# Kernel tuning notes

Measured on AMD Instinct MI355X. Metric: run time of the kernel, lower is better.

## Reference

```python
import jax, jax.numpy as jnp
import numpy as np

B, IN, HID, OUT, E = 8192, 1024, 4096, 1024, 8
EPS = 1e-5  # torch LayerNorm default


def _layernorm(x, gamma, beta):
    # normalize over last axis; gamma/beta broadcast as [E, dim] against [B, E, dim]
    mu = jnp.mean(x, axis=-1, keepdims=True)
    var = jnp.var(x, axis=-1, keepdims=True)
    return (x - mu) * jax.lax.rsqrt(var + EPS) * gamma + beta


def setup_inputs() -> dict:
    key = jax.random.key(0)
    ks = jax.random.split(key, 8)
    x = jax.random.normal(ks[0], (B, IN), dtype=jnp.float32)
    weights = jax.random.uniform(ks[1], (B, E), dtype=jnp.float32)
    s1 = 1.0 / np.sqrt(IN)
    s2 = 1.0 / np.sqrt(HID)
    W1 = jax.random.uniform(ks[2], (E, IN, HID), minval=-s1, maxval=s1, dtype=jnp.float32)
    b1 = jax.random.uniform(ks[3], (E, HID), minval=-s1, maxval=s1, dtype=jnp.float32)
    W2 = jax.random.uniform(ks[4], (E, HID, OUT), minval=-s2, maxval=s2, dtype=jnp.float32)
    b2 = jax.random.uniform(ks[5], (E, OUT), minval=-s2, maxval=s2, dtype=jnp.float32)
    g1 = jnp.ones((E, HID), dtype=jnp.float32)
    be1 = jnp.zeros((E, HID), dtype=jnp.float32)
    g2 = jnp.ones((E, OUT), dtype=jnp.float32)
    be2 = jnp.zeros((E, OUT), dtype=jnp.float32)
    return {"x": x, "weights": weights, "W1": W1, "b1": b1, "g1": g1, "be1": be1,
            "W2": W2, "b2": b2, "g2": g2, "be2": be2}


def reference(x, weights, W1, b1, g1, be1, W2, b2, g2, be2):
    # Each expert MLP([1024,4096,1024]): Linear -> LN -> GELU -> Linear -> LN -> GELU
    # (MLP appends LayerNorm + activation after EVERY Linear, including the last).
    # Dropout p=0 / eval mode -> identity. All experts run on every token.
    h = jnp.einsum('bi,eih->beh', x, W1) + b1          # [B, E, HID]
    h = jax.nn.gelu(_layernorm(h, g1, be1), approximate=False)
    y = jnp.einsum('beh,eho->beo', h, W2) + b2         # [B, E, OUT]
    y = jax.nn.gelu(_layernorm(y, g2, be2), approximate=False)
    # weighted combine: einsum('bij,bi->bj')
    return jnp.einsum('beo,be->bo', y, weights)        # [B, OUT]
```

## Files before the change

kernel.cpp:

```cpp
#include <hip/hip_runtime.h>
#include <cstdint>
#include <cstddef>

typedef unsigned short u16;
typedef float f32x4 __attribute__((ext_vector_type(4)));
typedef __bf16 bf16x8 __attribute__((ext_vector_type(8)));

#define B_DIM   8192
#define IN_DIM  1024
#define HID_DIM 4096
#define OUT_DIM 1024
#define NEXP    8

__device__ __forceinline__ u16 f2b(float f) {
    uint32_t u = __builtin_bit_cast(uint32_t, f);
    u += 0x7fffu + ((u >> 16) & 1u);
    return (u16)(u >> 16);
}
__device__ __forceinline__ float b2f(u16 b) {
    uint32_t u = ((uint32_t)b) << 16;
    return __builtin_bit_cast(float, u);
}
__device__ __forceinline__ float gelu_fast(float x) {
    float y = x * (0.7978845608f + 0.03567740814f * x * x);
    float a = fminf(y * 2.8853900818f, 80.0f);
    float e = __builtin_amdgcn_exp2f(a);
    return x * e * __builtin_amdgcn_rcpf(e + 1.0f);
}
__device__ __forceinline__ void async_cp16(const void* g, void* l) {
    __builtin_amdgcn_global_load_lds(
        (const __attribute__((address_space(1))) void*)g,
        (__attribute__((address_space(3))) void*)l,
        16, 0, 0);
}

__global__ __launch_bounds__(256)
void cvt_bf16(const float* __restrict__ in, u16* __restrict__ out, int n4) {
    int i = blockIdx.x * 256 + threadIdx.x;
    if (i >= n4) return;
    float4 v = *(const float4*)&in[(size_t)i * 4];
    uint2 o;
    o.x = (uint32_t)f2b(v.x) | ((uint32_t)f2b(v.y) << 16);
    o.y = (uint32_t)f2b(v.z) | ((uint32_t)f2b(v.w) << 16);
    *(uint2*)&out[(size_t)i * 4] = o;
}

__global__ __launch_bounds__(256)
void transpose_cvt2(const float* __restrict__ W1e, u16* __restrict__ w1t,
                    const float* __restrict__ W2e, u16* __restrict__ w2t) {
    __shared__ float tile[32][33];
    const float* W; u16* Wt; int K, N, n0, k0;
    if (blockIdx.z == 0) {
        W = W1e; Wt = w1t; K = IN_DIM; N = HID_DIM;
        n0 = blockIdx.x * 32; k0 = blockIdx.y * 32;
    } else {
        W = W2e; Wt = w2t; K = HID_DIM; N = OUT_DIM;
        n0 = blockIdx.y * 32; k0 = blockIdx.x * 32;
    }
    const int tx = threadIdx.x & 31, ty = threadIdx.x >> 5;
#pragma unroll
    for (int i = 0; i < 4; ++i) {
        int k = k0 + ty + i * 8;
        tile[ty + i * 8][tx] = W[(size_t)k * N + n0 + tx];
    }
    __syncthreads();
#pragma unroll
    for (int i = 0; i < 4; ++i) {
        int n = n0 + ty + i * 8;
        Wt[(size_t)n * K + k0 + tx] = f2b(tile[tx][ty + i * 8]);
    }
}

__global__ __launch_bounds__(256)
void gemm_bt_bias(const u16* __restrict__ A, const u16* __restrict__ Bt,
                  const float* __restrict__ bias, u16* __restrict__ C,
                  int M, int N, int K) {
    __shared__ __attribute__((aligned(16))) u16 sA[2][128 * 32];
    __shared__ __attribute__((aligned(16))) u16 sB[2][128 * 32];

    const int tid  = threadIdx.x;
    const int wid  = tid >> 6;
    const int lane = tid & 63;
    const int quad = lane >> 4;
    const int lr   = lane & 15;
    const int wm   = wid & 1;
    const int wn   = wid >> 1;

    const int NX = gridDim.x, NY = gridDim.y;
    const int bid = blockIdx.y * NX + blockIdx.x;
    const int xcd = bid & 7;
    const int j   = bid >> 3;
    const int yl  = j / NX;
    const int bx  = j - yl * NX;
    const int by  = xcd * (NY >> 3) + yl;

    const int m0 = by * 128;
    const int n0 = bx * 128;

    const int sr  = lane >> 2;
    const int scl = ((lane & 3) ^ ((lane >> 3) & 3)) * 8;
    const int qsw = (lr >> 1) & 3;

    const u16* Ag = A + (size_t)m0 * K;
    const u16* Bg = Bt + (size_t)n0 * K;

    f32x4 acc[4][4] = {};

    for (int k0 = 0; k0 < K; k0 += 64) {
#pragma unroll
        for (int s = 0; s < 2; ++s) {
#pragma unroll
            for (int i = 0; i < 2; ++i) {
                const int rb = wid * 32 + i * 16;
                async_cp16(Ag + (size_t)(rb + sr) * K + k0 + s * 32 + scl,
                           &sA[s][rb * 32]);
                async_cp16(Bg + (size_t)(rb + sr) * K + k0 + s * 32 + scl,
                           &sB[s][rb * 32]);
            }
        }
        __syncthreads();

#pragma unroll
        for (int s = 0; s < 2; ++s) {
            bf16x8 af[4], bfr[4];
#pragma unroll
            for (int mi = 0; mi < 4; ++mi)
                af[mi] = *(const bf16x8*)
                    &sA[s][(wm * 64 + mi * 16 + lr) * 32 + ((quad ^ qsw) * 8)];
#pragma unroll
            for (int ni = 0; ni < 4; ++ni)
                bfr[ni] = *(const bf16x8*)
                    &sB[s][(wn * 64 + ni * 16 + lr) * 32 + ((quad ^ qsw) * 8)];

#pragma unroll
            for (int mi = 0; mi < 4; ++mi)
#pragma unroll
                for (int ni = 0; ni < 4; ++ni)
                    acc[mi][ni] = __builtin_amdgcn_mfma_f32_16x16x32_bf16(
                        af[mi], bfr[ni], acc[mi][ni], 0, 0, 0);
        }

        __syncthreads();
    }

    float bvv[4];
#pragma unroll
    for (int ni = 0; ni < 4; ++ni)
        bvv[ni] = bias[n0 + wn * 64 + ni * 16 + lr];

#pragma unroll
    for (int mi = 0; mi < 4; ++mi) {
        const int mr = m0 + wm * 64 + mi * 16 + quad * 4;
#pragma unroll
        for (int r = 0; r < 4; ++r) {
            u16* Crow = C + (size_t)(mr + r) * N + n0 + wn * 64 + lr;
#pragma unroll
            for (int ni = 0; ni < 4; ++ni)
                Crow[ni * 16] = f2b(acc[mi][ni][r] + bvv[ni]);
        }
    }
}

__global__ __launch_bounds__(256)
void ln_gelu_hid(u16* __restrict__ h, const float* __restrict__ g,
                 const float* __restrict__ be) {
    __shared__ float red[8];
    const int row = blockIdx.x;
    u16* hp = h + (size_t)row * HID_DIM;
    const int t = threadIdx.x;

    uint4 v0 = *(const uint4*)&hp[t * 8];
    uint4 v1 = *(const uint4*)&hp[(t + 256) * 8];

    float vals[16];
    {
        const uint32_t w0[4] = {v0.x, v0.y, v0.z, v0.w};
        const uint32_t w1[4] = {v1.x, v1.y, v1.z, v1.w};
#pragma unroll
        for (int q = 0; q < 4; ++q) {
            vals[q * 2]     = b2f((u16)(w0[q] & 0xffffu));
            vals[q * 2 + 1] = b2f((u16)(w0[q] >> 16));
            vals[8 + q * 2]     = b2f((u16)(w1[q] & 0xffffu));
            vals[8 + q * 2 + 1] = b2f((u16)(w1[q] >> 16));
        }
    }
    float s = 0.f, ss = 0.f;
#pragma unroll
    for (int i = 0; i < 16; ++i) { s += vals[i]; ss += vals[i] * vals[i]; }

    float4 gv[4], bv[4];
    gv[0] = *(const float4*)&g[t * 8];
    gv[1] = *(const float4*)&g[t * 8 + 4];
    gv[2] = *(const float4*)&g[(t + 256) * 8];
    gv[3] = *(const float4*)&g[(t + 256) * 8 + 4];
    bv[0] = *(const float4*)&be[t * 8];
    bv[1] = *(const float4*)&be[t * 8 + 4];
    bv[2] = *(const float4*)&be[(t + 256) * 8];
    bv[3] = *(const float4*)&be[(t + 256) * 8 + 4];

#pragma unroll
    for (int off = 32; off > 0; off >>= 1) {
        s += __shfl_down(s, off, 64);
        ss += __shfl_down(ss, off, 64);
    }
    if ((t & 63) == 0) { red[(t >> 6) * 2] = s; red[(t >> 6) * 2 + 1] = ss; }
    __syncthreads();
    s  = red[0] + red[2] + red[4] + red[6];
    ss = red[1] + red[3] + red[5] + red[7];
    const float mean = s * (1.f / HID_DIM);
    const float rstd = rsqrtf(ss * (1.f / HID_DIM) - mean * mean + 1e-5f);

    const float* gf = (const float*)gv;
    const float* bf = (const float*)bv;
#pragma unroll
    for (int j = 0; j < 2; ++j) {
        uint4 o;
        uint32_t* ow = (uint32_t*)&o;
#pragma unroll
        for (int q = 0; q < 4; ++q) {
            const int k = j * 8 + q * 2;
            float u0 = gelu_fast((vals[k]     - mean) * rstd * gf[k]     + bf[k]);
            float u1 = gelu_fast((vals[k + 1] - mean) * rstd * gf[k + 1] + bf[k + 1]);
            ow[q] = (uint32_t)f2b(u0) | ((uint32_t)f2b(u1) << 16);
        }
        *(uint4*)&hp[(t + j * 256) * 8] = o;
    }
}

__global__ __launch_bounds__(256)
void ln_gelu_combine(const u16* __restrict__ y, const float* __restrict__ g,
                     const float* __restrict__ be, const float* __restrict__ wts,
                     float* __restrict__ out, int e, int first) {
    __shared__ float red[8];
    const int row = blockIdx.x;
    const u16* yp = y + (size_t)row * OUT_DIM;
    const int t = threadIdx.x;

    uint2 v = *(const uint2*)&yp[t * 4];
    float f0 = b2f((u16)(v.x & 0xffffu)), f1 = b2f((u16)(v.x >> 16));
    float f2 = b2f((u16)(v.y & 0xffffu)), f3 = b2f((u16)(v.y >> 16));
    float s = f0 + f1 + f2 + f3;
    float ss = f0 * f0 + f1 * f1 + f2 * f2 + f3 * f3;

    const int n = t * 4;
    float4 gv = *(const float4*)&g[n];
    float4 bvv = *(const float4*)&be[n];

#pragma unroll
    for (int off = 32; off > 0; off >>= 1) {
        s += __shfl_down(s, off, 64);
        ss += __shfl_down(ss, off, 64);
    }
    if ((t & 63) == 0) { red[(t >> 6) * 2] = s; red[(t >> 6) * 2 + 1] = ss; }
    __syncthreads();
    s  = red[0] + red[2] + red[4] + red[6];
    ss = red[1] + red[3] + red[5] + red[7];
    const float mean = s * (1.f / OUT_DIM);
    const float rstd = rsqrtf(ss * (1.f / OUT_DIM) - mean * mean + 1e-5f);

    const float w = wts[(size_t)row * NEXP + e];
    float4 o;
    if (first) { o.x = o.y = o.z = o.w = 0.f; }
    else       { o = *(const float4*)&out[(size_t)row * OUT_DIM + n]; }
    o.x += w * gelu_fast((f0 - mean) * rstd * gv.x + bvv.x);
    o.y += w * gelu_fast((f1 - mean) * rstd * gv.y + bvv.y);
    o.z += w * gelu_fast((f2 - mean) * rstd * gv.z + bvv.z);
    o.w += w * gelu_fast((f3 - mean) * rstd * gv.w + bvv.w);
    *(float4*)&out[(size_t)row * OUT_DIM + n] = o;
}

extern "C" void kernel_launch(void* const* d_in, const int* in_sizes, int n_in,
                              void* d_out, int out_size, void* d_ws, size_t ws_size,
                              hipStream_t stream) {
    (void)in_sizes; (void)n_in; (void)out_size; (void)ws_size;
    const float* x   = (const float*)d_in[0];
    const float* wts = (const float*)d_in[1];
    const float* W1  = (const float*)d_in[2];
    const float* b1  = (const float*)d_in[3];
    const float* g1  = (const float*)d_in[4];
    const float* be1 = (const float*)d_in[5];
    const float* W2  = (const float*)d_in[6];
    const float* b2  = (const float*)d_in[7];
    const float* g2  = (const float*)d_in[8];
    const float* be2 = (const float*)d_in[9];
    float* out = (float*)d_out;

    char* p = (char*)d_ws;
    u16* xb  = (u16*)p; p += (size_t)B_DIM * IN_DIM * 2;
    u16* w1t = (u16*)p; p += (size_t)HID_DIM * IN_DIM * 2;
    u16* w2t = (u16*)p; p += (size_t)OUT_DIM * HID_DIM * 2;
    u16* h   = (u16*)p; p += (size_t)B_DIM * HID_DIM * 2;
    u16* y   = (u16*)p; p += (size_t)B_DIM * OUT_DIM * 2;

    cvt_bf16<<<(B_DIM * IN_DIM / 4 + 255) / 256, 256, 0, stream>>>(x, xb, B_DIM * IN_DIM / 4);

    for (int e = 0; e < NEXP; ++e) {
        transpose_cvt2<<<dim3(HID_DIM / 32, IN_DIM / 32, 2), 256, 0, stream>>>(
            W1 + (size_t)e * IN_DIM * HID_DIM, w1t,
            W2 + (size_t)e * HID_DIM * OUT_DIM, w2t);
        gemm_bt_bias<<<dim3(HID_DIM / 128, B_DIM / 128), 256, 0, stream>>>(
            xb, w1t, b1 + (size_t)e * HID_DIM, h, B_DIM, HID_DIM, IN_DIM);
        ln_gelu_hid<<<B_DIM, 256, 0, stream>>>(h, g1 + (size_t)e * HID_DIM,
                                               be1 + (size_t)e * HID_DIM);
        gemm_bt_bias<<<dim3(OUT_DIM / 128, B_DIM / 128), 256, 0, stream>>>(
            h, w2t, b2 + (size_t)e * OUT_DIM, y, B_DIM, OUT_DIM, HID_DIM);
        ln_gelu_combine<<<B_DIM, 256, 0, stream>>>(y, g2 + (size_t)e * OUT_DIM,
                                                   be2 + (size_t)e * OUT_DIM, wts, out,
                                                   e, e == 0 ? 1 : 0);
    }
}
```

Baseline: 1.936 ms.

## Add 256x256-tile bf16 GEMM with 4-stage async pipeline for first layer

Adds a new GEMM kernel for the first expert layer that uses 256x256 output tiles, 512 threads and a four-buffer async copy pipeline with split A/B staging interleaved between MFMA phases. It also remaps block IDs to group row tiles per XCD and swizzles the LDS layout to reduce bank conflicts. The goal is more operand reuse per byte loaded and better overlap of global loads with matrix math. In exchange it raises LDS use (128 KB) and register pressure, which limits occupancy to one block per CU. The second GEMM still uses the old 128-tile kernel.

Result: faster. 1.887 ms (-2.6%).

```diff
diff --git a/kernel.cpp b/kernel.cpp
--- a/kernel.cpp
+++ b/kernel.cpp
@@ -68,6 +68,128 @@
     for (int i = 0; i < 4; ++i) {
         int n = n0 + ty + i * 8;
         Wt[(size_t)n * K + k0 + tx] = f2b(tile[tx][ty + i * 8]);
+    }
+}
+
+__global__ __launch_bounds__(512)
+void gemm256_bt_bias(const u16* __restrict__ A, const u16* __restrict__ Bt,
+                     const float* __restrict__ bias, u16* __restrict__ C,
+                     int M, int N, int K) {
+    __shared__ __attribute__((aligned(16))) u16 sA[4][256 * 32];
+    __shared__ __attribute__((aligned(16))) u16 sB[4][256 * 32];
+
+    const int tid  = threadIdx.x;
+    const int wid  = tid >> 6;
+    const int lane = tid & 63;
+    const int quad = lane >> 4;
+    const int lr   = lane & 15;
+    const int wm   = wid >> 2;
+    const int wn   = wid & 3;
+
+    const int NX = gridDim.x, NY = gridDim.y;
+    const int bid = blockIdx.y * NX + blockIdx.x;
+    const int xcd = bid & 7;
+    const int j   = bid >> 3;
+    const int yl  = j / NX;
+    const int bx  = j - yl * NX;
+    const int by  = xcd * (NY >> 3) + yl;
+
+    const int m0 = by * 256;
+    const int n0 = bx * 256;
+
+    const int sr  = lane >> 2;
+    const int scl = ((lane & 3) ^ ((lane >> 3) & 3)) * 8;
+    const int qsw = (lr >> 1) & 3;
+
+    const u16* Agr = A  + ((size_t)m0 + wid * 16 + sr) * (size_t)K + scl;
+    const u16* Bgr = Bt + ((size_t)n0 + wid * 16 + sr) * (size_t)K + scl;
+
+    const int NT = K >> 5;
+
+#pragma unroll
+    for (int t = 0; t < 3; ++t) {
+        const int kk = t * 32;
+        async_cp16(Agr + kk,                   &sA[t][wid * 512]);
+        async_cp16(Agr + (size_t)128 * K + kk, &sA[t][4096 + wid * 512]);
+        async_cp16(Bgr + kk,                   &sB[t][wid * 512]);
+        async_cp16(Bgr + (size_t)128 * K + kk, &sB[t][4096 + wid * 512]);
+    }
+    asm volatile("s_waitcnt vmcnt(8)" ::: "memory");
+    __builtin_amdgcn_s_barrier();
+    __builtin_amdgcn_sched_barrier(0);
+
+    f32x4 acc[8][4] = {};
+
+    for (int t = 0; t < NT; ++t) {
+        const u16* sa = sA[t & 3];
+        const u16* sb = sB[t & 3];
+        const int  pre = t + 3;
+        const bool stg = pre < NT;
+        const int  pb  = pre & 3;
+        const int  kk  = pre * 32;
+
+        bf16x8 af[4], bfr[4];
+#pragma unroll
+        for (int mi = 0; mi < 4; ++mi)
+            af[mi] = *(const bf16x8*)
+                &sa[(wm * 128 + mi * 16 + lr) * 32 + ((quad ^ qsw) * 8)];
+#pragma unroll
+        for (int ni = 0; ni < 4; ++ni)
+            bfr[ni] = *(const bf16x8*)
+                &sb[(wn * 64 + ni * 16 + lr) * 32 + ((quad ^ qsw) * 8)];
+        if (stg) {
+            async_cp16(Agr + kk,                   &sA[pb][wid * 512]);
+            async_cp16(Agr + (size_t)128 * K + kk, &sA[pb][4096 + wid * 512]);
+        }
+        __builtin_amdgcn_s_barrier();
+        __builtin_amdgcn_s_setprio(1);
+#pragma unroll
+        for (int mi = 0; mi < 4; ++mi)
+#pragma unroll
+            for (int ni = 0; ni < 4; ++ni)
+                acc[mi][ni] = __builtin_amdgcn_mfma_f32_16x16x32_bf16(
+                    af[mi], bfr[ni], acc[mi][ni], 0, 0, 0);
+        __builtin_amdgcn_s_setprio(0);
+        __builtin_amdgcn_s_barrier();
+
+#pragma unroll
+        for (int mi = 0; mi < 4; ++mi)
+            af[mi] = *(const bf16x8*)
+                &sa[(wm * 128 + (mi + 4) * 16 + lr) * 32 + ((quad ^ qsw) * 8)];
+        if (stg) {
+            async_cp16(Bgr + kk,                   &sB[pb][wid * 512]);
+            async_cp16(Bgr + (size_t)128 * K + kk, &sB[pb][4096 + wid * 512]);
+        }
+        __builtin_amdgcn_s_barrier();
+        __builtin_amdgcn_s_setprio(1);
+#pragma unroll
+        for (int mi = 0; mi < 4; ++mi)
+#pragma unroll
+            for (int ni = 0; ni < 4; ++ni)
+                acc[mi + 4][ni] = __builtin_amdgcn_mfma_f32_16x16x32_bf16(
+                    af[mi], bfr[ni], acc[mi + 4][ni], 0, 0, 0);
+        __builtin_amdgcn_s_setprio(0);
+        if (stg) asm volatile("s_waitcnt vmcnt(8)" ::: "memory");
+        else     asm volatile("s_waitcnt vmcnt(0)" ::: "memory");
+        __builtin_amdgcn_s_barrier();
+        __builtin_amdgcn_sched_barrier(0);
+    }
+
+    float bvv[4];
+#pragma unroll
+    for (int ni = 0; ni < 4; ++ni)
+        bvv[ni] = bias[n0 + wn * 64 + ni * 16 + lr];
+
+#pragma unroll
+    for (int mi = 0; mi < 8; ++mi) {
+        const int mr = m0 + wm * 128 + mi * 16 + quad * 4;
+#pragma unroll
+        for (int r = 0; r < 4; ++r) {
+            u16* Crow = C + (size_t)(mr + r) * N + n0 + wn * 64 + lr;
+#pragma unroll
+            for (int ni = 0; ni < 4; ++ni)
+                Crow[ni * 16] = f2b(acc[mi][ni][r] + bvv[ni]);
+        }
     }
 }
 
@@ -298,7 +420,7 @@
         transpose_cvt2<<<dim3(HID_DIM / 32, IN_DIM / 32, 2), 256, 0, stream>>>(
             W1 + (size_t)e * IN_DIM * HID_DIM, w1t,
             W2 + (size_t)e * HID_DIM * OUT_DIM, w2t);
-        gemm_bt_bias<<<dim3(HID_DIM / 128, B_DIM / 128), 256, 0, stream>>>(
+        gemm256_bt_bias<<<dim3(HID_DIM / 256, B_DIM / 256), 512, 0, stream>>>(
             xb, w1t, b1 + (size_t)e * HID_DIM, h, B_DIM, HID_DIM, IN_DIM);
         ln_gelu_hid<<<B_DIM, 256, 0, stream>>>(h, g1 + (size_t)e * HID_DIM,
                                                be1 + (size_t)e * HID_DIM);
```

## Use 256x256 four-stage pipelined GEMM and split-K for second expert GEMM

Applied to the files above, without the earlier changes.

Adds a new bf16 MFMA GEMM with 256x256 tiles, 512 threads, a 4-deep async-copy LDS pipeline and double-buffered register fragments, and uses it for the first expert GEMM. When the workspace is large enough, the second GEMM runs as a 2-way split-K with fp32 partial outputs. A new LN/GELU/combine kernel sums the two partials and the bias. The aim is more data reuse per tile and more blocks for the small-N second GEMM, at the cost of extra fp32 partial traffic and heavier register and LDS use.

Measured after the change: 1.936 ms. Within noise of the previous version (+0.0%).

```diff
diff --git a/kernel.cpp b/kernel.cpp
--- a/kernel.cpp
+++ b/kernel.cpp
@@ -71,6 +71,144 @@
     }
 }
 
+template<int F32OUT>
+__global__ __launch_bounds__(512, 2)
+void gemm256_pipe(const u16* __restrict__ A, const u16* __restrict__ Bt,
+                  const float* __restrict__ bias, void* __restrict__ Cv,
+                  int M, int N, int lda, int ldb, int Ksl) {
+    __shared__ __attribute__((aligned(16))) u16 sA[4][256 * 32];
+    __shared__ __attribute__((aligned(16))) u16 sB[4][256 * 32];
+
+    const int tid  = threadIdx.x;
+    const int wid  = tid >> 6;
+    const int lane = tid & 63;
+    const int quad = lane >> 4;
+    const int lr   = lane & 15;
+    const int wm   = wid >> 2;
+    const int wn   = wid & 3;
+    const int z    = blockIdx.z;
+
+    const int NX = gridDim.x, NY = gridDim.y;
+    const int bid = blockIdx.y * NX + blockIdx.x;
+    const int xcd = bid & 7;
+    const int j   = bid >> 3;
+    const int yl  = j / NX;
+    const int bx  = j - yl * NX;
+    const int by  = xcd * (NY >> 3) + yl;
+
+    const int m0 = by * 256;
+    const int n0 = bx * 256;
+
+    const int sr  = lane >> 2;
+    const int scl = ((lane & 3) ^ ((lane >> 3) & 3)) * 8;
+    const int qsw = (lr >> 1) & 3;
+
+    const u16* Ag0 = A  + ((size_t)z * Ksl) + ((size_t)m0 + wid * 16 + sr) * (size_t)lda + scl;
+    const u16* Ag1 = Ag0 + (size_t)128 * lda;
+    const u16* Bg0 = Bt + ((size_t)z * Ksl) + ((size_t)n0 + wid * 16 + sr) * (size_t)ldb + scl;
+    const u16* Bg1 = Bg0 + (size_t)128 * ldb;
+
+    const int rdA = (wm * 128 + lr) * 32 + ((quad ^ qsw) * 8);
+    const int rdB = (wn * 64  + lr) * 32 + ((quad ^ qsw) * 8);
+
+    const int NT = Ksl >> 5;
+
+#define STAGE(tt) do {                                                        \
+        const int sl_ = (tt) & 3;                                             \
+        const size_t ko_ = (size_t)(tt) * 32;                                 \
+        async_cp16(Ag0 + ko_, &sA[sl_][wid * 512]);                           \
+        async_cp16(Ag1 + ko_, &sA[sl_][4096 + wid * 512]);                    \
+        async_cp16(Bg0 + ko_, &sB[sl_][wid * 512]);                           \
+        async_cp16(Bg1 + ko_, &sB[sl_][4096 + wid * 512]);                    \
+    } while (0)
+
+#define READF(afd, bfd, tt) do {                                              \
+        const u16* sa_ = &sA[(tt) & 3][0];                                    \
+        const u16* sb_ = &sB[(tt) & 3][0];                                    \
+        _Pragma("unroll")                                                     \
+        for (int mi = 0; mi < 8; ++mi)                                        \
+            afd[mi] = *(const bf16x8*)&sa_[rdA + mi * 512];                   \
+        _Pragma("unroll")                                                     \
+        for (int ni = 0; ni < 4; ++ni)                                        \
+            bfd[ni] = *(const bf16x8*)&sb_[rdB + ni * 512];                   \
+    } while (0)
+
+#define CLUSTER(afc, bfc) do {                                                \
+        __builtin_amdgcn_s_setprio(1);                                        \
+        _Pragma("unroll")                                                     \
+        for (int mi = 0; mi < 8; ++mi)                                        \
+            _Pragma("unroll")                                                 \
+            for (int ni = 0; ni < 4; ++ni)                                    \
+                acc[mi][ni] = __builtin_amdgcn_mfma_f32_16x16x32_bf16(        \
+                    afc[mi], bfc[ni], acc[mi][ni], 0, 0, 0);                  \
+        __builtin_amdgcn_s_setprio(0);                                        \
+    } while (0)
+
+#define BODY(tt, afc, bfc, afn, bfn) do {                                     \
+        const int pre_ = (tt) + 3;                                            \
+        if (pre_ < NT) STAGE(pre_);                                           \
+        READF(afn, bfn, (tt) + 1);                                            \
+        CLUSTER(afc, bfc);                                                    \
+        if (pre_ < NT) asm volatile("s_waitcnt vmcnt(4)" ::: "memory");       \
+        else           asm volatile("s_waitcnt vmcnt(0)" ::: "memory");       \
+        asm volatile("s_barrier" ::: "memory");                               \
+    } while (0)
+
+    STAGE(0); STAGE(1); STAGE(2);
+    asm volatile("s_waitcnt vmcnt(4)" ::: "memory");
+    asm volatile("s_barrier" ::: "memory");
+
+    bf16x8 afA[8], bfA[4], afB[8], bfB[4];
+    READF(afA, bfA, 0);
+
+    f32x4 acc[8][4] = {};
+
+#pragma unroll 1
+    for (int t = 0; t < NT - 2; t += 2) {
+        BODY(t,     afA, bfA, afB, bfB);
+        BODY(t + 1, afB, bfB, afA, bfA);
+    }
+    BODY(NT - 2, afA, bfA, afB, bfB);
+    CLUSTER(afB, bfB);
+
+#undef BODY
+#undef CLUSTER
+#undef READF
+#undef STAGE
+
+    if constexpr (F32OUT) {
+        float* C = (float*)Cv + (size_t)z * ((size_t)M * N);
+#pragma unroll
+        for (int mi = 0; mi < 8; ++mi) {
+            const int mr = m0 + wm * 128 + mi * 16 + quad * 4;
+#pragma unroll
+            for (int r = 0; r < 4; ++r) {
+                float* Crow = C + (size_t)(mr + r) * N + n0 + wn * 64 + lr;
+#pragma unroll
+                for (int ni = 0; ni < 4; ++ni)
+                    Crow[ni * 16] = acc[mi][ni][r];
+            }
+        }
+    } else {
+        u16* C = (u16*)Cv;
+        float bvv[4];
+#pragma unroll
+        for (int ni = 0; ni < 4; ++ni)
+            bvv[ni] = bias[n0 + wn * 64 + ni * 16 + lr];
+#pragma unroll
+        for (int mi = 0; mi < 8; ++mi) {
+            const int mr = m0 + wm * 128 + mi * 16 + quad * 4;
+#pragma unroll
+            for (int r = 0; r < 4; ++r) {
+                u16* Crow = C + (size_t)(mr + r) * N + n0 + wn * 64 + lr;
+#pragma unroll
+                for (int ni = 0; ni < 4; ++ni)
+                    Crow[ni * 16] = f2b(acc[mi][ni][r] + bvv[ni]);
+            }
+        }
+    }
+}
+
 __global__ __launch_bounds__(256)
 void gemm_bt_bias(const u16* __restrict__ A, const u16* __restrict__ Bt,
                   const float* __restrict__ bias, u16* __restrict__ C,
@@ -269,10 +407,56 @@
     *(float4*)&out[(size_t)row * OUT_DIM + n] = o;
 }
 
+__global__ __launch_bounds__(256)
+void ln_gelu_combine_f32(const float* __restrict__ P, const float* __restrict__ g,
+                         const float* __restrict__ be, const float* __restrict__ bs,
+                         const float* __restrict__ wts, float* __restrict__ out,
+                         int e, int first) {
+    __shared__ float red[8];
+    const int row = blockIdx.x;
+    const int t = threadIdx.x;
+    const int n = t * 4;
+
+    const float* p0 = P + (size_t)row * OUT_DIM + n;
+    const float* p1 = p0 + (size_t)B_DIM * OUT_DIM;
+    float4 a  = *(const float4*)p0;
+    float4 b  = *(const float4*)p1;
+    float4 c  = *(const float4*)&bs[n];
+    float f0 = a.x + b.x + c.x, f1 = a.y + b.y + c.y;
+    float f2 = a.z + b.z + c.z, f3 = a.w + b.w + c.w;
+    float s = f0 + f1 + f2 + f3;
+    float ss = f0 * f0 + f1 * f1 + f2 * f2 + f3 * f3;
+
+    float4 gv = *(const float4*)&g[n];
+    float4 bvv = *(const float4*)&be[n];
+
+#pragma unroll
+    for (int off = 32; off > 0; off >>= 1) {
+        s += __shfl_down(s, off, 64);
+        ss += __shfl_down(ss, off, 64);
+    }
+    if ((t & 63) == 0) { red[(t >> 6) * 2] = s; red[(t >> 6) * 2 + 1] = ss; }
+    __syncthreads();
+    s  = red[0] + red[2] + red[4] + red[6];
+    ss = red[1] + red[3] + red[5] + red[7];
+    const float mean = s * (1.f / OUT_DIM);
+    const float rstd = rsqrtf(ss * (1.f / OUT_DIM) - mean * mean + 1e-5f);
+
+    const float w = wts[(size_t)row * NEXP + e];
+    float4 o;
+    if (first) { o.x = o.y = o.z = o.w = 0.f; }
+    else       { o = *(const float4*)&out[(size_t)row * OUT_DIM + n]; }
+    o.x += w * gelu_fast((f0 - mean) * rstd * gv.x + bvv.x);
+    o.y += w * gelu_fast((f1 - mean) * rstd * gv.y + bvv.y);
+    o.z += w * gelu_fast((f2 - mean) * rstd * gv.z + bvv.z);
+    o.w += w * gelu_fast((f3 - mean) * rstd * gv.w + bvv.w);
+    *(float4*)&out[(size_t)row * OUT_DIM + n] = o;
+}
+
 extern "C" void kernel_launch(void* const* d_in, const int* in_sizes, int n_in,
                               void* d_out, int out_size, void* d_ws, size_t ws_size,
                               hipStream_t stream) {
-    (void)in_sizes; (void)n_in; (void)out_size; (void)ws_size;
+    (void)in_sizes; (void)n_in; (void)out_size;
     const float* x   = (const float*)d_in[0];
     const float* wts = (const float*)d_in[1];
     const float* W1  = (const float*)d_in[2];
@@ -290,7 +474,13 @@
     u16* w1t = (u16*)p; p += (size_t)HID_DIM * IN_DIM * 2;
     u16* w2t = (u16*)p; p += (size_t)OUT_DIM * HID_DIM * 2;
     u16* h   = (u16*)p; p += (size_t)B_DIM * HID_DIM * 2;
-    u16* y   = (u16*)p; p += (size_t)B_DIM * OUT_DIM * 2;
+    float* P = (float*)p;
+    u16*  y  = (u16*)p;
+
+    const size_t need = (size_t)B_DIM * IN_DIM * 2 + (size_t)HID_DIM * IN_DIM * 2 +
+                        (size_t)OUT_DIM * HID_DIM * 2 + (size_t)B_DIM * HID_DIM * 2 +
+                        (size_t)2 * B_DIM * OUT_DIM * 4;
+    const int splitk = (ws_size >= need) ? 1 : 0;
 
     cvt_bf16<<<(B_DIM * IN_DIM / 4 + 255) / 256, 256, 0, stream>>>(x, xb, B_DIM * IN_DIM / 4);
 
@@ -298,14 +488,22 @@
         transpose_cvt2<<<dim3(HID_DIM / 32, IN_DIM / 32, 2), 256, 0, stream>>>(
             W1 + (size_t)e * IN_DIM * HID_DIM, w1t,
             W2 + (size_t)e * HID_DIM * OUT_DIM, w2t);
-        gemm_bt_bias<<<dim3(HID_DIM / 128, B_DIM / 128), 256, 0, stream>>>(
-            xb, w1t, b1 + (size_t)e * HID_DIM, h, B_DIM, HID_DIM, IN_DIM);
+        gemm256_pipe<0><<<dim3(HID_DIM / 256, B_DIM / 256, 1), 512, 0, stream>>>(
+            xb, w1t, b1 + (size_t)e * HID_DIM, h, B_DIM, HID_DIM, IN_DIM, IN_DIM, IN_DIM);
         ln_gelu_hid<<<B_DIM, 256, 0, stream>>>(h, g1 + (size_t)e * HID_DIM,
                                                be1 + (size_t)e * HID_DIM);
-        gemm_bt_bias<<<dim3(OUT_DIM / 128, B_DIM / 128), 256, 0, stream>>>(
-            h, w2t, b2 + (size_t)e * OUT_DIM, y, B_DIM, OUT_DIM, HID_DIM);
-        ln_gelu_combine<<<B_DIM, 256, 0, stream>>>(y, g2 + (size_t)e * OUT_DIM,
-                                                   be2 + (size_t)e * OUT_DIM, wts, out,
-                                                   e, e == 0 ? 1 : 0);
-    }
-}
+        if (splitk) {
+            gemm256_pipe<1><<<dim3(OUT_DIM / 256, B_DIM / 256, 2), 512, 0, stream>>>(
+                h, w2t, nullptr, P, B_DIM, OUT_DIM, HID_DIM, HID_DIM, HID_DIM / 2);
+            ln_gelu_combine_f32<<<B_DIM, 256, 0, stream>>>(
+                P, g2 + (size_t)e * OUT_DIM, be2 + (size_t)e * OUT_DIM,
+                b2 + (size_t)e * OUT_DIM, wts, out, e, e == 0 ? 1 : 0);
+        } else {
+            gemm_bt_bias<<<dim3(OUT_DIM / 128, B_DIM / 128), 256, 0, stream>>>(
+                h, w2t, b2 + (size_t)e * OUT_DIM, y, B_DIM, OUT_DIM, HID_DIM);
+            ln_gelu_combine<<<B_DIM, 256, 0, stream>>>(y, g2 + (size_t)e * OUT_DIM,
+                                                       be2 + (size_t)e * OUT_DIM, wts, out,
+                                                       e, e == 0 ? 1 : 0);
+        }
+    }
+}
```
